# Performance work log

Measured on AMD Instinct MI355X. Metric: run time of the kernel, lower is better.

Reference implementation:

```python
import jax, jax.numpy as jnp
import numpy as np

N = 16384          # tokens (batch*seq)
D = 2048           # input_dim
H = 2 * D          # router hidden dim
E = 64             # num_experts
NUM_SHARED = 8
TOP_K = 2


def setup_inputs() -> dict:
    key = jax.random.key(0)
    k_x, k_w1, k_b1, k_w2, k_b2 = jax.random.split(key, 5)
    s1 = 1.0 / np.sqrt(D)
    s2 = 1.0 / np.sqrt(H)
    return {
        "x": jax.random.normal(k_x, (N, D), dtype=jnp.float32),
        "W1": jax.random.uniform(k_w1, (D, H), jnp.float32, -s1, s1),
        "b1": jax.random.uniform(k_b1, (H,), jnp.float32, -s1, s1),
        "W2": jax.random.uniform(k_w2, (H, E), jnp.float32, -s2, s2),
        "b2": jax.random.uniform(k_b2, (E,), jnp.float32, -s2, s2),
    }


def reference(x, W1, b1, W2, b2):
    # router MLP: linear -> exact (erf) GELU -> linear -> softmax
    h = jax.nn.gelu(x @ W1 + b1, approximate=False)          # [N, H]
    weights = jax.nn.softmax(h @ W2 + b2, axis=-1)            # [N, E]
    global_weights = weights[:, :NUM_SHARED]                  # [N, num_shared]
    local = weights[:, NUM_SHARED:]                           # [N, E - num_shared]
    local_weights, local_indices = jax.lax.top_k(local, TOP_K)  # [N, top_k] each
    return (global_weights, local_weights, local_indices, weights)
```

## Files before the change

### kernel.cpp

```cpp
#include <hip/hip_runtime.h>
#include <math.h>

namespace {
constexpr int kN = 16384;
constexpr int kD = 2048;
constexpr int kH = 4096;
constexpr int kE = 64;
constexpr int kShared = 8;

constexpr int OFF_GW = 0;
constexpr int OFF_LW = kN * kShared;
constexpr int OFF_LI = OFF_LW + kN * 2;
constexpr int OFF_W  = OFF_LI + kN * 2;

constexpr int GS_STRIDE = 132;
constexpr int HSPLIT = 4;
constexpr int CHUNKS = 8;

constexpr size_t XH_OFF  = 0;
constexpr size_t XL_OFF  = (size_t)kN * kD;
constexpr size_t W1TH_OFF = XL_OFF + (size_t)kN * kD;
constexpr size_t W1TL_OFF = W1TH_OFF + (size_t)kH * kD;
constexpr size_t WS_BASE = (W1TL_OFF + (size_t)kH * kD) * 2;
constexpr size_t PART_FLOAT_OFF = WS_BASE / 4;
constexpr size_t WS_FULL = WS_BASE + (size_t)HSPLIT * kN * kE * 4;
}

typedef _Float16 half8  __attribute__((ext_vector_type(8)));
typedef _Float16 half4t __attribute__((ext_vector_type(4)));
typedef float    f32x16 __attribute__((ext_vector_type(16)));

__device__ __forceinline__ void async16(const _Float16* g, _Float16* l) {
    __builtin_amdgcn_global_load_lds(
        (const __attribute__((address_space(1))) void*)g,
        (__attribute__((address_space(3))) void*)l, 16, 0, 0);
}

__global__ __launch_bounds__(256)
void convert_x(const float* __restrict__ x, _Float16* __restrict__ xh,
               _Float16* __restrict__ xl)
{
    const size_t i = ((size_t)blockIdx.x * 256 + threadIdx.x) * 4;
    const float4 v = *reinterpret_cast<const float4*>(x + i);
    half4t h, l;
    const float vs[4] = {v.x, v.y, v.z, v.w};
    #pragma unroll
    for (int j = 0; j < 4; ++j) {
        const _Float16 hj = (_Float16)vs[j];
        h[j] = hj;
        l[j] = (_Float16)((vs[j] - (float)hj) * 2048.0f);
    }
    *reinterpret_cast<half4t*>(xh + i) = h;
    *reinterpret_cast<half4t*>(xl + i) = l;
}

__global__ __launch_bounds__(256)
void convert_w1t(const float* __restrict__ W1, _Float16* __restrict__ th,
                 _Float16* __restrict__ tl)
{
    __shared__ float T[64][65];
    const int bk = blockIdx.x & 31;
    const int bn = blockIdx.x >> 5;
    const int k0 = bk * 64, n0 = bn * 64;
    const int t = threadIdx.x;
    const int c4 = (t & 15) * 4, r = t >> 4;

    #pragma unroll
    for (int i = 0; i < 4; ++i) {
        const int kk = r + 16 * i;
        const float4 v = *reinterpret_cast<const float4*>(
            W1 + (size_t)(k0 + kk) * kH + n0 + c4);
        T[kk][c4 + 0] = v.x; T[kk][c4 + 1] = v.y;
        T[kk][c4 + 2] = v.z; T[kk][c4 + 3] = v.w;
    }
    __syncthreads();
    #pragma unroll
    for (int i = 0; i < 4; ++i) {
        const int nn = r + 16 * i;
        half4t h, l;
        #pragma unroll
        for (int j = 0; j < 4; ++j) {
            const float vv = T[c4 + j][nn];
            const _Float16 hj = (_Float16)vv;
            h[j] = hj;
            l[j] = (_Float16)((vv - (float)hj) * 2048.0f);
        }
        *reinterpret_cast<half4t*>(th + (size_t)(n0 + nn) * kD + k0 + c4) = h;
        *reinterpret_cast<half4t*>(tl + (size_t)(n0 + nn) * kD + k0 + c4) = l;
    }
}

__global__ __launch_bounds__(256, 2)
void gemm1_mfma(const _Float16* __restrict__ xh, const float* __restrict__ b1,
                const float* __restrict__ W2, float* __restrict__ dst,
                int atomicMode)
{
    __shared__ __align__(16) float smem[64 * GS_STRIDE];
    _Float16* lds = (_Float16*)smem;
    float* gS = smem;

    const int t = threadIdx.x;
    const int lane = t & 63;
    const int w = t >> 6;
    const int bx = blockIdx.x;
    const int hSplit = bx & 3;
    const int rowBlock = bx >> 2;
    const int rowBase = rowBlock * 128;

    const int mw = (w >> 1) * 64, nw = (w & 1) * 64;

    unsigned int gofsA[4], gofsB[4];
    #pragma unroll
    for (int i = 0; i < 8; ++i) {
        const int c = i * 256 + t;
        const int tile = c >> 9;
        const int s = c & 511;
        const int row = s >> 2;
        const int pq = s & 3;
        const int q = pq ^ (row & 3) ^ ((row >> 2) & 3);
        const unsigned int plane =
            (tile == 0) ? (unsigned int)XH_OFF :
            (tile == 1) ? (unsigned int)XL_OFF :
            (tile == 2) ? (unsigned int)W1TH_OFF : (unsigned int)W1TL_OFF;
        if (tile < 2)
            gofsA[i] = plane + (unsigned int)(rowBase + row) * kD + q * 8;
        else
            gofsB[i - 4] = plane + (unsigned int)row * kD + q * 8;
    }

    int aOff[2][2], bOff[2][2];
    #pragma unroll
    for (int mt = 0; mt < 2; ++mt)
        #pragma unroll
        for (int ks = 0; ks < 2; ++ks) {
            const int row = mw + mt * 32 + (lane & 31);
            const int q = (lane >> 5) + 2 * ks;
            aOff[mt][ks] = row * 32 + ((q ^ (row & 3) ^ ((row >> 2) & 3)) * 8);
        }
    #pragma unroll
    for (int nt = 0; nt < 2; ++nt)
        #pragma unroll
        for (int ks = 0; ks < 2; ++ks) {
            const int row = nw + nt * 32 + (lane & 31);
            const int q = (lane >> 5) + 2 * ks;
            bOff[nt][ks] = row * 32 + ((q ^ (row & 3) ^ ((row >> 2) & 3)) * 8);
        }

    const int g_r0 = (t >> 3) * 4;
    const int g_e0 = (t & 7) * 8;
    float lacc[4][8];
    #pragma unroll
    for (int i = 0; i < 4; ++i)
        #pragma unroll
        for (int j = 0; j < 8; ++j) lacc[i][j] = 0.0f;

    for (int chunk = 0; chunk < CHUNKS; ++chunk) {
        const int hBase = hSplit * (CHUNKS * 128) + chunk * 128;
        const unsigned int hOff = (unsigned int)hBase * kD;

        f32x16 accH[2][2], accL[2][2];
        #pragma unroll
        for (int a = 0; a < 2; ++a)
            #pragma unroll
            for (int b = 0; b < 2; ++b)
                #pragma unroll
                for (int r = 0; r < 16; ++r) { accH[a][b][r] = 0.0f; accL[a][b][r] = 0.0f; }

        for (int kt = 0; kt < kD; kt += 32) {
            __syncthreads();
            #pragma unroll
            for (int i = 0; i < 4; ++i)
                async16(xh + gofsA[i] + kt, lds + ((i * 256 + t) * 8));
            #pragma unroll
            for (int i = 0; i < 4; ++i)
                async16(xh + gofsB[i] + hOff + kt, lds + (((i + 4) * 256 + t) * 8));
            __syncthreads();

            half8 aH[2][2], aL[2][2], bH[2][2], bL[2][2];
            #pragma unroll
            for (int mt = 0; mt < 2; ++mt)
                #pragma unroll
                for (int ks = 0; ks < 2; ++ks) {
                    aH[mt][ks] = *reinterpret_cast<const half8*>(lds + aOff[mt][ks]);
                    aL[mt][ks] = *reinterpret_cast<const half8*>(lds + 4096 + aOff[mt][ks]);
                }
            #pragma unroll
            for (int nt = 0; nt < 2; ++nt)
                #pragma unroll
                for (int ks = 0; ks < 2; ++ks) {
                    bH[nt][ks] = *reinterpret_cast<const half8*>(lds + 8192 + bOff[nt][ks]);
                    bL[nt][ks] = *reinterpret_cast<const half8*>(lds + 12288 + bOff[nt][ks]);
                }

            #pragma unroll
            for (int ks = 0; ks < 2; ++ks)
                #pragma unroll
                for (int mt = 0; mt < 2; ++mt)
                    #pragma unroll
                    for (int nt = 0; nt < 2; ++nt) {
                        accH[mt][nt] = __builtin_amdgcn_mfma_f32_32x32x16_f16(
                            aH[mt][ks], bH[nt][ks], accH[mt][nt], 0, 0, 0);
                        accL[mt][nt] = __builtin_amdgcn_mfma_f32_32x32x16_f16(
                            aH[mt][ks], bL[nt][ks], accL[mt][nt], 0, 0, 0);
                        accL[mt][nt] = __builtin_amdgcn_mfma_f32_32x32x16_f16(
                            aL[mt][ks], bH[nt][ks], accL[mt][nt], 0, 0, 0);
                    }
        }

        const float inv2048 = 1.0f / 2048.0f;
        for (int hf = 0; hf < 2; ++hf) {
            __syncthreads();
            if ((w & 1) == hf) {
                #pragma unroll
                for (int nt = 0; nt < 2; ++nt) {
                    const int hl = nt * 32 + (lane & 31);
                    const float bb = b1[hBase + hf * 64 + hl];
                    #pragma unroll
                    for (int mt = 0; mt < 2; ++mt) {
                        #pragma unroll
                        for (int rq = 0; rq < 4; ++rq) {
                            float vr[4];
                            #pragma unroll
                            for (int rr = 0; rr < 4; ++rr) {
                                const int r = rq * 4 + rr;
                                const float hv = accH[mt][nt][r] + accL[mt][nt][r] * inv2048 + bb;
                                vr[rr] = 0.5f * hv * (1.0f + erff(hv * 0.70710678118654752f));
                            }
                            const int mrow = mw + mt * 32 + 8 * rq + 4 * (lane >> 5);
                            *reinterpret_cast<float4*>(gS + hl * GS_STRIDE + mrow) =
                                make_float4(vr[0], vr[1], vr[2], vr[3]);
                        }
                    }
                }
            }
            __syncthreads();
            const float* W2p = W2 + (size_t)(hBase + hf * 64) * kE + g_e0;
            #pragma unroll 4
            for (int h = 0; h < 64; ++h) {
                const float4 gv = *reinterpret_cast<const float4*>(gS + h * GS_STRIDE + g_r0);
                const float4 w0 = *reinterpret_cast<const float4*>(W2p + (size_t)h * kE);
                const float4 w1 = *reinterpret_cast<const float4*>(W2p + (size_t)h * kE + 4);
                const float ga[4] = {gv.x, gv.y, gv.z, gv.w};
                const float wb[8] = {w0.x, w0.y, w0.z, w0.w, w1.x, w1.y, w1.z, w1.w};
                #pragma unroll
                for (int i = 0; i < 4; ++i)
                    #pragma unroll
                    for (int j = 0; j < 8; ++j)
                        lacc[i][j] = fmaf(ga[i], wb[j], lacc[i][j]);
            }
        }
    }

    if (atomicMode) {
        #pragma unroll
        for (int i = 0; i < 4; ++i)
            #pragma unroll
            for (int j = 0; j < 8; ++j)
                atomicAdd(dst + (size_t)(rowBase + g_r0 + i) * kE + g_e0 + j, lacc[i][j]);
    } else {
        float* drow = dst + ((size_t)hSplit * kN + rowBase + g_r0) * kE + g_e0;
        #pragma unroll
        for (int i = 0; i < 4; ++i) {
            *reinterpret_cast<float4*>(drow + (size_t)i * kE) =
                make_float4(lacc[i][0], lacc[i][1], lacc[i][2], lacc[i][3]);
            *reinterpret_cast<float4*>(drow + (size_t)i * kE + 4) =
                make_float4(lacc[i][4], lacc[i][5], lacc[i][6], lacc[i][7]);
        }
    }
}

__global__ __launch_bounds__(256, 2)
void gemm1_kernel(const float* __restrict__ x, const float* __restrict__ W1,
                  const float* __restrict__ b1, const float* __restrict__ W2,
                  float* __restrict__ logits)
{
    __shared__ __align__(16) float smem[64 * GS_STRIDE];
    float* As = smem;
    float* Bs = smem + 32 * 128;
    float* gS = smem;

    const int t  = threadIdx.x;
    const int bx = blockIdx.x;
    const int rowBlock = bx >> 2;
    const int hSplit   = bx & 3;
    const int rowBase  = rowBlock * 128;
    const int hBase0   = hSplit * 1024;

    const int ty = t >> 4;
    const int tx = t & 15;
    const int r0 = ty * 8;
    const int c0 = tx * 8;
    const int g_r0 = (t >> 3) * 4;
    const int g_e0 = (t & 7) * 8;

    float lacc[4][8];
    #pragma unroll
    for (int i = 0; i < 4; ++i)
        #pragma unroll
        for (int j = 0; j < 8; ++j) lacc[i][j] = 0.0f;

    for (int chunk = 0; chunk < 8; ++chunk) {
        const int hBase = hBase0 + chunk * 128;
        float C[8][8];
        #pragma unroll
        for (int i = 0; i < 8; ++i)
            #pragma unroll
            for (int j = 0; j < 8; ++j) C[i][j] = 0.0f;

        for (int kt = 0; kt < kD; kt += 32) {
            __syncthreads();
            #pragma unroll
            for (int i = 0; i < 4; ++i) {
                const int f  = t + 256 * i;
                const int m  = f >> 3;
                const int kq = (f & 7) * 4;
                const float4 v = *reinterpret_cast<const float4*>(
                    x + (size_t)(rowBase + m) * kD + kt + kq);
                As[(kq + 0) * 128 + m] = v.x;
                As[(kq + 1) * 128 + m] = v.y;
                As[(kq + 2) * 128 + m] = v.z;
                As[(kq + 3) * 128 + m] = v.w;
            }
            #pragma unroll
            for (int i = 0; i < 4; ++i) {
                const int f  = t + 256 * i;
                const int k  = f >> 5;
                const int n4 = (f & 31) * 4;
                *reinterpret_cast<float4*>(Bs + k * 128 + n4) =
                    *reinterpret_cast<const float4*>(W1 + (size_t)(kt + k) * kH + hBase + n4);
            }
            __syncthreads();
            #pragma unroll 8
            for (int k = 0; k < 32; ++k) {
                const float4 a0 = *reinterpret_cast<const float4*>(As + k * 128 + r0);
                const float4 a1 = *reinterpret_cast<const float4*>(As + k * 128 + r0 + 4);
                const float4 b0 = *reinterpret_cast<const float4*>(Bs + k * 128 + c0);
                const float4 b1v = *reinterpret_cast<const float4*>(Bs + k * 128 + c0 + 4);
                const float a[8] = {a0.x, a0.y, a0.z, a0.w, a1.x, a1.y, a1.z, a1.w};
                const float b[8] = {b0.x, b0.y, b0.z, b0.w, b1v.x, b1v.y, b1v.z, b1v.w};
                #pragma unroll
                for (int i = 0; i < 8; ++i)
                    #pragma unroll
                    for (int j = 0; j < 8; ++j)
                        C[i][j] = fmaf(a[i], b[j], C[i][j]);
            }
        }

        #pragma unroll
        for (int j = 0; j < 8; ++j) {
            const float bb = b1[hBase + c0 + j];
            #pragma unroll
            for (int i = 0; i < 8; ++i) {
                const float hv = C[i][j] + bb;
                C[i][j] = 0.5f * hv * (1.0f + erff(hv * 0.70710678118654752f));
            }
        }

        for (int half = 0; half < 2; ++half) {
            __syncthreads();
            if ((tx >> 3) == half) {
                const int hloc0 = c0 - half * 64;
                #pragma unroll
                for (int j = 0; j < 8; ++j) {
                    const float4 col = make_float4(C[0][j], C[1][j], C[2][j], C[3][j]);
                    const float4 col2 = make_float4(C[4][j], C[5][j], C[6][j], C[7][j]);
                    *reinterpret_cast<float4*>(gS + (hloc0 + j) * GS_STRIDE + r0)     = col;
                    *reinterpret_cast<float4*>(gS + (hloc0 + j) * GS_STRIDE + r0 + 4) = col2;
                }
            }
            __syncthreads();
            const float* W2p = W2 + (size_t)(hBase + half * 64) * kE + g_e0;
            #pragma unroll 4
            for (int h = 0; h < 64; ++h) {
                const float4 gv = *reinterpret_cast<const float4*>(gS + h * GS_STRIDE + g_r0);
                const float4 w0 = *reinterpret_cast<const float4*>(W2p + (size_t)h * kE);
                const float4 w1 = *reinterpret_cast<const float4*>(W2p + (size_t)h * kE + 4);
                const float ga[4] = {gv.x, gv.y, gv.z, gv.w};
                const float wb[8] = {w0.x, w0.y, w0.z, w0.w, w1.x, w1.y, w1.z, w1.w};
                #pragma unroll
                for (int i = 0; i < 4; ++i)
                    #pragma unroll
                    for (int j = 0; j < 8; ++j)
                        lacc[i][j] = fmaf(ga[i], wb[j], lacc[i][j]);
            }
        }
    }

    #pragma unroll
    for (int i = 0; i < 4; ++i)
        #pragma unroll
        for (int j = 0; j < 8; ++j)
            atomicAdd(logits + (size_t)(rowBase + g_r0 + i) * kE + g_e0 + j, lacc[i][j]);
}

__global__ __launch_bounds__(256)
void router_kernel(const float* __restrict__ b2, const float* __restrict__ src,
                   int atomicMode, float* __restrict__ out)
{
    const int lane = threadIdx.x & 63;
    const int row  = blockIdx.x * 4 + (threadIdx.x >> 6);

    float logit;
    if (atomicMode) {
        logit = src[(size_t)row * kE + lane] + b2[lane];
    } else {
        const float* p = src + (size_t)row * kE + lane;
        logit = p[0] + p[(size_t)kN * kE] + p[(size_t)2 * kN * kE] +
                p[(size_t)3 * kN * kE] + b2[lane];
    }

    float m = logit;
    #pragma unroll
    for (int off = 32; off > 0; off >>= 1) m = fmaxf(m, __shfl_xor(m, off));
    const float p = expf(logit - m);
    float s = p;
    #pragma unroll
    for (int off = 32; off > 0; off >>= 1) s += __shfl_xor(s, off);
    const float w = p / s;

    out[OFF_W + (size_t)row * kE + lane] = w;
    if (lane < kShared) out[OFF_GW + (size_t)row * kShared + lane] = w;

    float v1 = (lane >= kShared) ? w : -1.0f;
    int   i1 = lane - kShared;
    #pragma unroll
    for (int off = 32; off > 0; off >>= 1) {
        const float ov = __shfl_xor(v1, off);
        const int   oi = __shfl_xor(i1, off);
        if (ov > v1 || (ov == v1 && oi < i1)) { v1 = ov; i1 = oi; }
    }
    float v2 = (lane >= kShared && (lane - kShared) != i1) ? w : -1.0f;
    int   i2 = lane - kShared;
    #pragma unroll
    for (int off = 32; off > 0; off >>= 1) {
        const float ov = __shfl_xor(v2, off);
        const int   oi = __shfl_xor(i2, off);
        if (ov > v2 || (ov == v2 && oi < i2)) { v2 = ov; i2 = oi; }
    }
    if (lane == 0) {
        out[OFF_LW + (size_t)row * 2 + 0] = v1;
        out[OFF_LW + (size_t)row * 2 + 1] = v2;
        out[OFF_LI + (size_t)row * 2 + 0] = (float)i1;
        out[OFF_LI + (size_t)row * 2 + 1] = (float)i2;
    }
}

extern "C" void kernel_launch(void* const* d_in, const int* in_sizes, int n_in,
                              void* d_out, int out_size, void* d_ws, size_t ws_size,
                              hipStream_t stream)
{
    const float* x  = (const float*)d_in[0];
    const float* W1 = (const float*)d_in[1];
    const float* b1 = (const float*)d_in[2];
    const float* W2 = (const float*)d_in[3];
    const float* b2 = (const float*)d_in[4];
    float* out = (float*)d_out;
    float* logits = out + OFF_W;

    if (ws_size >= WS_BASE) {
        _Float16* base = (_Float16*)d_ws;
        const int atomicMode = (ws_size >= WS_FULL) ? 0 : 1;
        float* dst = atomicMode ? logits : ((float*)d_ws + PART_FLOAT_OFF);
        if (atomicMode)
            hipMemsetAsync(logits, 0, (size_t)kN * kE * sizeof(float), stream);
        hipLaunchKernelGGL(convert_x, dim3(kN * kD / 1024), dim3(256), 0, stream,
                           x, base + XH_OFF, base + XL_OFF);
        hipLaunchKernelGGL(convert_w1t, dim3((kD / 64) * (kH / 64)), dim3(256), 0, stream,
                           W1, base + W1TH_OFF, base + W1TL_OFF);
        hipLaunchKernelGGL(gemm1_mfma, dim3((kN / 128) * HSPLIT), dim3(256), 0, stream,
                           base + XH_OFF, b1, W2, dst, atomicMode);
        hipLaunchKernelGGL(router_kernel, dim3(kN / 4), dim3(256), 0, stream,
                           b2, dst, atomicMode, out);
    } else {
        hipMemsetAsync(logits, 0, (size_t)kN * kE * sizeof(float), stream);
        hipLaunchKernelGGL(gemm1_kernel, dim3((kN / 128) * 4), dim3(256), 0, stream,
                           x, W1, b1, W2, logits);
        hipLaunchKernelGGL(router_kernel, dim3(kN / 4), dim3(256), 0, stream,
                           b2, logits, 1, out);
    }
}
```

Baseline: 1.334 ms.

## Halve MFMA GEMM row tile to 64 and raise occupancy to four blocks per CU

```diff
diff --git a/kernel.cpp b/kernel.cpp
--- a/kernel.cpp
+++ b/kernel.cpp
@@ -13,9 +13,9 @@
 constexpr int OFF_LI = OFF_LW + kN * 2;
 constexpr int OFF_W  = OFF_LI + kN * 2;
 
-constexpr int GS_STRIDE = 132;
 constexpr int HSPLIT = 4;
 constexpr int CHUNKS = 8;
+constexpr int GS_STRIDE = 68;
 
 constexpr size_t XH_OFF  = 0;
 constexpr size_t XL_OFF  = (size_t)kN * kD;
@@ -24,6 +24,10 @@
 constexpr size_t WS_BASE = (W1TL_OFF + (size_t)kH * kD) * 2;
 constexpr size_t PART_FLOAT_OFF = WS_BASE / 4;
 constexpr size_t WS_FULL = WS_BASE + (size_t)HSPLIT * kN * kE * 4;
+
+constexpr unsigned DXL = (unsigned)XL_OFF;
+constexpr unsigned DWL = (unsigned)(W1TL_OFF - W1TH_OFF);
+constexpr unsigned D64 = 64u * kD;
 }
 
 typedef _Float16 half8  __attribute__((ext_vector_type(8)));
@@ -90,12 +94,12 @@
     }
 }
 
-__global__ __launch_bounds__(256, 2)
+__global__ __launch_bounds__(256, 4)
 void gemm1_mfma(const _Float16* __restrict__ xh, const float* __restrict__ b1,
                 const float* __restrict__ W2, float* __restrict__ dst,
                 int atomicMode)
 {
-    __shared__ __align__(16) float smem[64 * GS_STRIDE];
+    __shared__ __align__(16) float smem[6144];
     _Float16* lds = (_Float16*)smem;
     float* gS = smem;
 
@@ -104,132 +108,90 @@
     const int w = t >> 6;
     const int bx = blockIdx.x;
     const int hSplit = bx & 3;
-    const int rowBlock = bx >> 2;
-    const int rowBase = rowBlock * 128;
-
-    const int mw = (w >> 1) * 64, nw = (w & 1) * 64;
-
-    unsigned int gofsA[4], gofsB[4];
-    #pragma unroll
-    for (int i = 0; i < 8; ++i) {
-        const int c = i * 256 + t;
-        const int tile = c >> 9;
-        const int s = c & 511;
-        const int row = s >> 2;
-        const int pq = s & 3;
-        const int q = pq ^ (row & 3) ^ ((row >> 2) & 3);
-        const unsigned int plane =
-            (tile == 0) ? (unsigned int)XH_OFF :
-            (tile == 1) ? (unsigned int)XL_OFF :
-            (tile == 2) ? (unsigned int)W1TH_OFF : (unsigned int)W1TL_OFF;
-        if (tile < 2)
-            gofsA[i] = plane + (unsigned int)(rowBase + row) * kD + q * 8;
-        else
-            gofsB[i - 4] = plane + (unsigned int)row * kD + q * 8;
-    }
-
-    int aOff[2][2], bOff[2][2];
-    #pragma unroll
-    for (int mt = 0; mt < 2; ++mt)
-        #pragma unroll
-        for (int ks = 0; ks < 2; ++ks) {
-            const int row = mw + mt * 32 + (lane & 31);
-            const int q = (lane >> 5) + 2 * ks;
-            aOff[mt][ks] = row * 32 + ((q ^ (row & 3) ^ ((row >> 2) & 3)) * 8);
-        }
-    #pragma unroll
-    for (int nt = 0; nt < 2; ++nt)
-        #pragma unroll
-        for (int ks = 0; ks < 2; ++ks) {
-            const int row = nw + nt * 32 + (lane & 31);
-            const int q = (lane >> 5) + 2 * ks;
-            bOff[nt][ks] = row * 32 + ((q ^ (row & 3) ^ ((row >> 2) & 3)) * 8);
-        }
-
-    const int g_r0 = (t >> 3) * 4;
+    const int rowBase = (bx >> 2) * 64;
+
+    const int mw = (w & 1) * 32;
+    const int nw = (w >> 1) * 64;
+
+    {
+    }
+    const int srow = t >> 2;
+    const int sq = (t & 3) ^ (srow & 3) ^ ((srow >> 2) & 3);
+    const unsigned gofsA0 = (unsigned)XH_OFF + (unsigned)(rowBase + srow) * kD + sq * 8;
+    const unsigned gofsB0 = (unsigned)W1TH_OFF + (unsigned)srow * kD + sq * 8;
+
+    const int ar = mw + (lane & 31);
+    const int aOff = ar * 32 + ((((lane >> 5)) ^ (ar & 3) ^ ((ar >> 2) & 3)) * 8);
+    const int br = nw + (lane & 31);
+    const int bOff = br * 32 + ((((lane >> 5)) ^ (br & 3) ^ ((br >> 2) & 3)) * 8);
+
+    const int g_r0 = (t >> 3) * 2;
     const int g_e0 = (t & 7) * 8;
-    float lacc[4][8];
-    #pragma unroll
-    for (int i = 0; i < 4; ++i)
+    float lacc[2][8];
+    #pragma unroll
+    for (int i = 0; i < 2; ++i)
         #pragma unroll
         for (int j = 0; j < 8; ++j) lacc[i][j] = 0.0f;
 
     for (int chunk = 0; chunk < CHUNKS; ++chunk) {
         const int hBase = hSplit * (CHUNKS * 128) + chunk * 128;
-        const unsigned int hOff = (unsigned int)hBase * kD;
-
-        f32x16 accH[2][2], accL[2][2];
-        #pragma unroll
-        for (int a = 0; a < 2; ++a)
-            #pragma unroll
-            for (int b = 0; b < 2; ++b)
-                #pragma unroll
-                for (int r = 0; r < 16; ++r) { accH[a][b][r] = 0.0f; accL[a][b][r] = 0.0f; }
+        const unsigned hOff = (unsigned)hBase * kD;
+
+        f32x16 accH[2], accL[2];
+        #pragma unroll
+        for (int b = 0; b < 2; ++b)
+            #pragma unroll
+            for (int r = 0; r < 16; ++r) { accH[b][r] = 0.0f; accL[b][r] = 0.0f; }
 
         for (int kt = 0; kt < kD; kt += 32) {
             __syncthreads();
-            #pragma unroll
-            for (int i = 0; i < 4; ++i)
-                async16(xh + gofsA[i] + kt, lds + ((i * 256 + t) * 8));
-            #pragma unroll
-            for (int i = 0; i < 4; ++i)
-                async16(xh + gofsB[i] + hOff + kt, lds + (((i + 4) * 256 + t) * 8));
-            __syncthreads();
-
-            half8 aH[2][2], aL[2][2], bH[2][2], bL[2][2];
-            #pragma unroll
-            for (int mt = 0; mt < 2; ++mt)
-                #pragma unroll
-                for (int ks = 0; ks < 2; ++ks) {
-                    aH[mt][ks] = *reinterpret_cast<const half8*>(lds + aOff[mt][ks]);
-                    aL[mt][ks] = *reinterpret_cast<const half8*>(lds + 4096 + aOff[mt][ks]);
-                }
-            #pragma unroll
-            for (int nt = 0; nt < 2; ++nt)
-                #pragma unroll
-                for (int ks = 0; ks < 2; ++ks) {
-                    bH[nt][ks] = *reinterpret_cast<const half8*>(lds + 8192 + bOff[nt][ks]);
-                    bL[nt][ks] = *reinterpret_cast<const half8*>(lds + 12288 + bOff[nt][ks]);
-                }
-
-            #pragma unroll
-            for (int ks = 0; ks < 2; ++ks)
-                #pragma unroll
-                for (int mt = 0; mt < 2; ++mt)
-                    #pragma unroll
-                    for (int nt = 0; nt < 2; ++nt) {
-                        accH[mt][nt] = __builtin_amdgcn_mfma_f32_32x32x16_f16(
-                            aH[mt][ks], bH[nt][ks], accH[mt][nt], 0, 0, 0);
-                        accL[mt][nt] = __builtin_amdgcn_mfma_f32_32x32x16_f16(
-                            aH[mt][ks], bL[nt][ks], accL[mt][nt], 0, 0, 0);
-                        accL[mt][nt] = __builtin_amdgcn_mfma_f32_32x32x16_f16(
-                            aL[mt][ks], bH[nt][ks], accL[mt][nt], 0, 0, 0);
-                    }
+            async16(xh + gofsA0 + kt,              lds + t * 8);
+            async16(xh + gofsA0 + DXL + kt,        lds + 2048 + t * 8);
+            async16(xh + gofsB0 + hOff + kt,       lds + 4096 + t * 8);
+            async16(xh + gofsB0 + D64 + hOff + kt, lds + 6144 + t * 8);
+            async16(xh + gofsB0 + DWL + hOff + kt, lds + 8192 + t * 8);
+            async16(xh + gofsB0 + DWL + D64 + hOff + kt, lds + 10240 + t * 8);
+            __syncthreads();
+
+            #pragma unroll
+            for (int ks = 0; ks < 2; ++ks) {
+                const int aO = aOff ^ (ks * 16);
+                const int bO = bOff ^ (ks * 16);
+                const half8 aH  = *reinterpret_cast<const half8*>(lds + aO);
+                const half8 aL  = *reinterpret_cast<const half8*>(lds + 2048 + aO);
+                const half8 bH0 = *reinterpret_cast<const half8*>(lds + 4096 + bO);
+                const half8 bH1 = *reinterpret_cast<const half8*>(lds + 5120 + bO);
+                const half8 bL0 = *reinterpret_cast<const half8*>(lds + 8192 + bO);
+                const half8 bL1 = *reinterpret_cast<const half8*>(lds + 9216 + bO);
+                accH[0] = __builtin_amdgcn_mfma_f32_32x32x16_f16(aH, bH0, accH[0], 0, 0, 0);
+                accL[0] = __builtin_amdgcn_mfma_f32_32x32x16_f16(aH, bL0, accL[0], 0, 0, 0);
+                accL[0] = __builtin_amdgcn_mfma_f32_32x32x16_f16(aL, bH0, accL[0], 0, 0, 0);
+                accH[1] = __builtin_amdgcn_mfma_f32_32x32x16_f16(aH, bH1, accH[1], 0, 0, 0);
+                accL[1] = __builtin_amdgcn_mfma_f32_32x32x16_f16(aH, bL1, accL[1], 0, 0, 0);
+                accL[1] = __builtin_amdgcn_mfma_f32_32x32x16_f16(aL, bH1, accL[1], 0, 0, 0);
+            }
         }
 
         const float inv2048 = 1.0f / 2048.0f;
         for (int hf = 0; hf < 2; ++hf) {
             __syncthreads();
-            if ((w & 1) == hf) {
+            if ((w >> 1) == hf) {
                 #pragma unroll
                 for (int nt = 0; nt < 2; ++nt) {
                     const int hl = nt * 32 + (lane & 31);
                     const float bb = b1[hBase + hf * 64 + hl];
                     #pragma unroll
-                    for (int mt = 0; mt < 2; ++mt) {
+                    for (int rq = 0; rq < 4; ++rq) {
+                        float vr[4];
                         #pragma unroll
-                        for (int rq = 0; rq < 4; ++rq) {
-                            float vr[4];
-                            #pragma unroll
-                            for (int rr = 0; rr < 4; ++rr) {
-                                const int r = rq * 4 + rr;
-                                const float hv = accH[mt][nt][r] + accL[mt][nt][r] * inv2048 + bb;
-                                vr[rr] = 0.5f * hv * (1.0f + erff(hv * 0.70710678118654752f));
-                            }
-                            const int mrow = mw + mt * 32 + 8 * rq + 4 * (lane >> 5);
-                            *reinterpret_cast<float4*>(gS + hl * GS_STRIDE + mrow) =
-                                make_float4(vr[0], vr[1], vr[2], vr[3]);
+                        for (int rr = 0; rr < 4; ++rr) {
+                            const int r = rq * 4 + rr;
+                            const float hv = accH[nt][r] + accL[nt][r] * inv2048 + bb;
+                            vr[rr] = 0.5f * hv * (1.0f + erff(hv * 0.70710678118654752f));
                         }
+                        const int mrow = mw + 8 * rq + 4 * (lane >> 5);
+                        *reinterpret_cast<float4*>(gS + hl * GS_STRIDE + mrow) =
+                            make_float4(vr[0], vr[1], vr[2], vr[3]);
                     }
                 }
             }
@@ -237,30 +199,29 @@
             const float* W2p = W2 + (size_t)(hBase + hf * 64) * kE + g_e0;
             #pragma unroll 4
             for (int h = 0; h < 64; ++h) {
-                const float4 gv = *reinterpret_cast<const float4*>(gS + h * GS_STRIDE + g_r0);
+                const float2 gv = *reinterpret_cast<const float2*>(gS + h * GS_STRIDE + g_r0);
                 const float4 w0 = *reinterpret_cast<const float4*>(W2p + (size_t)h * kE);
                 const float4 w1 = *reinterpret_cast<const float4*>(W2p + (size_t)h * kE + 4);
-                const float ga[4] = {gv.x, gv.y, gv.z, gv.w};
                 const float wb[8] = {w0.x, w0.y, w0.z, w0.w, w1.x, w1.y, w1.z, w1.w};
                 #pragma unroll
-                for (int i = 0; i < 4; ++i)
-                    #pragma unroll
-                    for (int j = 0; j < 8; ++j)
-                        lacc[i][j] = fmaf(ga[i], wb[j], lacc[i][j]);
+                for (int j = 0; j < 8; ++j) {
+                    lacc[0][j] = fmaf(gv.x, wb[j], lacc[0][j]);
+                    lacc[1][j] = fmaf(gv.y, wb[j], lacc[1][j]);
+                }
             }
         }
     }
 
     if (atomicMode) {
         #pragma unroll
-        for (int i = 0; i < 4; ++i)
+        for (int i = 0; i < 2; ++i)
             #pragma unroll
             for (int j = 0; j < 8; ++j)
                 atomicAdd(dst + (size_t)(rowBase + g_r0 + i) * kE + g_e0 + j, lacc[i][j]);
     } else {
         float* drow = dst + ((size_t)hSplit * kN + rowBase + g_r0) * kE + g_e0;
         #pragma unroll
-        for (int i = 0; i < 4; ++i) {
+        for (int i = 0; i < 2; ++i) {
             *reinterpret_cast<float4*>(drow + (size_t)i * kE) =
                 make_float4(lacc[i][0], lacc[i][1], lacc[i][2], lacc[i][3]);
             *reinterpret_cast<float4*>(drow + (size_t)i * kE + 4) =
@@ -274,7 +235,7 @@
                   const float* __restrict__ b1, const float* __restrict__ W2,
                   float* __restrict__ logits)
 {
-    __shared__ __align__(16) float smem[64 * GS_STRIDE];
+    __shared__ __align__(16) float smem[64 * 132];
     float* As = smem;
     float* Bs = smem + 32 * 128;
     float* gS = smem;
@@ -364,15 +325,15 @@
                 for (int j = 0; j < 8; ++j) {
                     const float4 col = make_float4(C[0][j], C[1][j], C[2][j], C[3][j]);
                     const float4 col2 = make_float4(C[4][j], C[5][j], C[6][j], C[7][j]);
-                    *reinterpret_cast<float4*>(gS + (hloc0 + j) * GS_STRIDE + r0)     = col;
-                    *reinterpret_cast<float4*>(gS + (hloc0 + j) * GS_STRIDE + r0 + 4) = col2;
+                    *reinterpret_cast<float4*>(gS + (hloc0 + j) * 132 + r0)     = col;
+                    *reinterpret_cast<float4*>(gS + (hloc0 + j) * 132 + r0 + 4) = col2;
                 }
             }
             __syncthreads();
             const float* W2p = W2 + (size_t)(hBase + half * 64) * kE + g_e0;
             #pragma unroll 4
             for (int h = 0; h < 64; ++h) {
-                const float4 gv = *reinterpret_cast<const float4*>(gS + h * GS_STRIDE + g_r0);
+                const float4 gv = *reinterpret_cast<const float4*>(gS + h * 132 + g_r0);
                 const float4 w0 = *reinterpret_cast<const float4*>(W2p + (size_t)h * kE);
                 const float4 w1 = *reinterpret_cast<const float4*>(W2p + (size_t)h * kE + 4);
                 const float ga[4] = {gv.x, gv.y, gv.z, gv.w};
@@ -467,7 +428,7 @@
                            x, base + XH_OFF, base + XL_OFF);
         hipLaunchKernelGGL(convert_w1t, dim3((kD / 64) * (kH / 64)), dim3(256), 0, stream,
                            W1, base + W1TH_OFF, base + W1TL_OFF);
-        hipLaunchKernelGGL(gemm1_mfma, dim3((kN / 128) * HSPLIT), dim3(256), 0, stream,
+        hipLaunchKernelGGL(gemm1_mfma, dim3((kN / 64) * HSPLIT), dim3(256), 0, stream,
                            base + XH_OFF, b1, W2, dst, atomicMode);
         hipLaunchKernelGGL(router_kernel, dim3(kN / 4), dim3(256), 0, stream,
                            b2, dst, atomicMode, out);
```

After: 1.595 ms. 19.5% more time.
